# Kernel tuning notes

Hardware: AMD Instinct MI355X
Metric: run time of the kernel (lower is better)

The kernel has to match this reference:

```python
import jax, jax.numpy as jnp
import numpy as np

N = 50000
E = 400000


def _cheb_norm(edge_index, dtype):
    # PyG ChebConv norm (normalization='sym', lambda_max=2.0):
    # remove self loops, L_hat = -D^{-1/2} A D^{-1/2} on off-diagonal edges.
    src, dst = edge_index[0], edge_index[1]
    mask = (src != dst).astype(dtype)
    deg = jax.ops.segment_sum(mask, src, num_segments=N)
    dinv = jnp.where(deg > 0, jax.lax.rsqrt(jnp.where(deg > 0, deg, 1.0)), 0.0)
    w = -dinv[src] * dinv[dst] * mask  # [E]
    return src, dst, w


def _cheb_conv(x, src, dst, w, W0, W1, b):
    # out = T0(x) W0 + T1(x) W1 + b, T0 = x, T1 = L_hat x
    tx1 = jax.ops.segment_sum(w[:, None] * x[src], dst, num_segments=N)
    return x @ W0 + tx1 @ W1 + b


def setup_inputs() -> dict:
    key = jax.random.key(0)
    ks = jax.random.split(key, 12)
    s = 0.05
    inp = {
        "x": jax.random.normal(ks[0], (N, 128), dtype=jnp.float32),
        "edge_index": jax.random.randint(ks[1], (2, E), 0, N, dtype=jnp.int64),
        "W1_0": jax.random.normal(ks[2], (128, 256), dtype=jnp.float32) * s,
        "W1_1": jax.random.normal(ks[3], (128, 256), dtype=jnp.float32) * s,
        "b1": jnp.zeros((256,), dtype=jnp.float32),
        "W2_0": jax.random.normal(ks[4], (256, 256), dtype=jnp.float32) * s,
        "W2_1": jax.random.normal(ks[5], (256, 256), dtype=jnp.float32) * s,
        "b2": jnp.zeros((256,), dtype=jnp.float32),
        "W3_0": jax.random.normal(ks[6], (256, 256), dtype=jnp.float32) * s,
        "W3_1": jax.random.normal(ks[7], (256, 256), dtype=jnp.float32) * s,
        "b3": jnp.zeros((256,), dtype=jnp.float32),
    }
    return inp


def reference(x, edge_index, W1_0, W1_1, b1, W2_0, W2_1, b2, W3_0, W3_1, b3):
    # Eval mode: F.dropout with training=False is identity, so dropout is omitted.
    src, dst, w = _cheb_norm(edge_index, x.dtype)
    h = jax.nn.relu(_cheb_conv(x, src, dst, w, W1_0, W1_1, b1))
    h = jax.nn.relu(_cheb_conv(h, src, dst, w, W2_0, W2_1, b2))
    h = _cheb_conv(h, src, dst, w, W3_0, W3_1, b3)
    return h
```

## Files before the change

### kernel.cpp

```cpp
#include <hip/hip_runtime.h>
#include <hip/hip_bf16.h>


typedef __attribute__((ext_vector_type(8))) short bf16x8;
typedef __attribute__((ext_vector_type(4))) float f32x4;

__device__ __forceinline__ float bf2f(unsigned int lo16) {
    unsigned int t = lo16 << 16;
    return __builtin_bit_cast(float, t);
}
__device__ __forceinline__ unsigned short f2bf(float f) {
    unsigned int u = __builtin_bit_cast(unsigned int, f);
    unsigned int r = (u + 0x7fffu + ((u >> 16) & 1u)) >> 16;
    return (unsigned short)r;
}

__global__ __launch_bounds__(256) void deg_cnt_kernel(const int* __restrict__ src,
                                                      const int* __restrict__ dst,
                                                      float* __restrict__ deg,
                                                      int* __restrict__ cnt, int E) {
    int e = blockIdx.x * blockDim.x + threadIdx.x;
    if (e < E) {
        int s = src[e], d = dst[e];
        if (s != d) atomicAdd(&deg[s], 1.0f);
        atomicAdd(&cnt[d], 1);
    }
}

__global__ __launch_bounds__(256) void dinv_kernel(float* __restrict__ deg, int N) {
    int i = blockIdx.x * blockDim.x + threadIdx.x;
    if (i < N) {
        float d = deg[i];
        deg[i] = (d > 0.0f) ? rsqrtf(d) : 0.0f;
    }
}

__global__ __launch_bounds__(256) void scan_partial(const int* __restrict__ cnt,
                                                    int* __restrict__ part, int N) {
    __shared__ int lds[256];
    int tid = threadIdx.x;
    int base = blockIdx.x * 1024 + tid * 4;
    int s = 0;
    #pragma unroll
    for (int i = 0; i < 4; ++i) if (base + i < N) s += cnt[base + i];
    lds[tid] = s;
    __syncthreads();
    for (int off = 128; off > 0; off >>= 1) {
        if (tid < off) lds[tid] += lds[tid + off];
        __syncthreads();
    }
    if (tid == 0) part[blockIdx.x] = lds[0];
}

__global__ __launch_bounds__(64) void scan_small(int* __restrict__ part, int NB,
                                                 int* __restrict__ rowptr, int N) {
    if (threadIdx.x == 0 && blockIdx.x == 0) {
        int total = 0;
        for (int i = 0; i < NB; ++i) { int t = part[i]; part[i] = total; total += t; }
        rowptr[N] = total;
    }
}

__global__ __launch_bounds__(256) void scan_chunk(const int* __restrict__ cnt,
                                                  const int* __restrict__ part,
                                                  int* __restrict__ rowptr, int N) {
    __shared__ int lds[256];
    int tid = threadIdx.x;
    int base = blockIdx.x * 1024 + tid * 4;
    int c[4];
    #pragma unroll
    for (int i = 0; i < 4; ++i) c[i] = (base + i < N) ? cnt[base + i] : 0;
    int ts = c[0] + c[1] + c[2] + c[3];
    lds[tid] = ts;
    __syncthreads();
    for (int off = 1; off < 256; off <<= 1) {
        int v = (tid >= off) ? lds[tid - off] : 0;
        __syncthreads();
        lds[tid] += v;
        __syncthreads();
    }
    int o = part[blockIdx.x] + lds[tid] - ts;
    #pragma unroll
    for (int i = 0; i < 4; ++i) {
        if (base + i < N) rowptr[base + i] = o;
        o += c[i];
    }
}

__global__ __launch_bounds__(256) void fill_kernel(const int* __restrict__ src,
                                                   const int* __restrict__ dst,
                                                   const float* __restrict__ dinv,
                                                   int* __restrict__ cursor,
                                                   int* __restrict__ esrc,
                                                   float* __restrict__ ew, int E) {
    int e = blockIdx.x * blockDim.x + threadIdx.x;
    if (e < E) {
        int s = src[e], d = dst[e];
        int pos = atomicAdd(&cursor[d], 1);
        esrc[pos] = s;
        ew[pos] = (s != d) ? (-dinv[s] * dinv[d]) : 0.0f;
    }
}

__global__ __launch_bounds__(256) void cast_x_kernel(const float* __restrict__ x,
                                                     unsigned short* __restrict__ xb,
                                                     long long n4) {
    long long i = (long long)blockIdx.x * 256 + threadIdx.x;
    if (i >= n4) return;
    float4 v = reinterpret_cast<const float4*>(x)[i];
    ushort4 o;
    o.x = f2bf(v.x); o.y = f2bf(v.y); o.z = f2bf(v.z); o.w = f2bf(v.w);
    reinterpret_cast<ushort4*>(xb)[i] = o;
}

struct TParams {
    const float* W[6];
    unsigned short* WT[6];
    int K[6];
};
__global__ __launch_bounds__(256) void transpose_cast_all(TParams p) {
    int m = blockIdx.z;
    int K = p.K[m];
    int kb = blockIdx.x * 32, nb = blockIdx.y * 32;
    if (kb >= K) return;
    const float* W = p.W[m];
    unsigned short* WT = p.WT[m];
    __shared__ float t[32][33];
    int lx = threadIdx.x & 31, ly = threadIdx.x >> 5;
    #pragma unroll
    for (int i = 0; i < 32; i += 8)
        t[ly + i][lx] = W[(size_t)(kb + ly + i) * 256 + nb + lx];
    __syncthreads();
    #pragma unroll
    for (int i = 0; i < 32; i += 8)
        WT[(size_t)(nb + ly + i) * K + kb + lx] = f2bf(t[lx][ly + i]);
}

template <int F>
__global__ __launch_bounds__(256) void gather_bf16(const int* __restrict__ rowptr,
                                                   const int* __restrict__ esrc,
                                                   const float* __restrict__ ew,
                                                   const unsigned short* __restrict__ xb,
                                                   unsigned short* __restrict__ txb,
                                                   int N) {
    constexpr int V = F / 64;
    int wave = threadIdx.x >> 6, lane = threadIdx.x & 63;
    int n = blockIdx.x * 4 + wave;
    if (n >= N) return;
    int beg = rowptr[n], end = rowptr[n + 1];
    float acc[V] = {};
    int s_next = 0; float w_next = 0.0f;
    if (beg < end) { s_next = esrc[beg]; w_next = ew[beg]; }
    for (int k = beg; k < end; ++k) {
        int s = s_next; float wv = w_next;
        if (k + 1 < end) { s_next = esrc[k + 1]; w_next = ew[k + 1]; }
        const unsigned short* p = &xb[(size_t)s * F + lane * V];
        if (V == 2) {
            unsigned int u = *reinterpret_cast<const unsigned int*>(p);
            acc[0] += wv * bf2f(u & 0xffffu);
            acc[1] += wv * bf2f(u >> 16);
        } else {
            uint2 u = *reinterpret_cast<const uint2*>(p);
            acc[0] += wv * bf2f(u.x & 0xffffu);
            acc[1] += wv * bf2f(u.x >> 16);
            acc[2] += wv * bf2f(u.y & 0xffffu);
            acc[3] += wv * bf2f(u.y >> 16);
        }
    }
    unsigned short* q = &txb[(size_t)n * F + lane * V];
    if (V == 2) {
        unsigned int o = (unsigned int)f2bf(acc[0]) | ((unsigned int)f2bf(acc[1]) << 16);
        *reinterpret_cast<unsigned int*>(q) = o;
    } else {
        uint2 o;
        o.x = (unsigned int)f2bf(acc[0]) | ((unsigned int)f2bf(acc[1]) << 16);
        o.y = (unsigned int)f2bf(acc[2]) | ((unsigned int)f2bf(acc[3]) << 16);
        *reinterpret_cast<uint2*>(q) = o;
    }
}

template <int K, bool RELU, typename OutT>
__global__ __launch_bounds__(256, 3) void gemm_mfma(const unsigned short* __restrict__ Xb,
                                                    const unsigned short* __restrict__ Tb,
                                                    const unsigned short* __restrict__ W0T,
                                                    const unsigned short* __restrict__ W1T,
                                                    const float* __restrict__ bias,
                                                    OutT* __restrict__ out, int M) {
    constexpr int SA = 72;
    __shared__ unsigned short As[64 * SA];
    __shared__ unsigned short Bs[256 * SA];

    const int tid = threadIdx.x;
    const int wave = tid >> 6;
    const int lane = tid & 63;
    const int l15 = lane & 15;
    const int quad = lane >> 4;
    const int row0 = blockIdx.x * 64;

    const int srow = tid >> 3;
    const int scol = (tid & 7) * 8;

    f32x4 acc[4][4];
    #pragma unroll
    for (int i = 0; i < 4; ++i)
        #pragma unroll
        for (int j = 0; j < 4; ++j) acc[i][j] = (f32x4){0.f, 0.f, 0.f, 0.f};

    #pragma unroll
    for (int pass = 0; pass < 2; ++pass) {
        const unsigned short* Amat = pass ? Tb : Xb;
        const unsigned short* Wmat = pass ? W1T : W0T;
        for (int k0 = 0; k0 < K; k0 += 64) {
            if (pass != 0 || k0 != 0) __syncthreads();
            #pragma unroll
            for (int r = 0; r < 2; ++r) {
                int row = r * 32 + srow;
                int grow = row0 + row; if (grow > M - 1) grow = M - 1;
                uint4 v = *reinterpret_cast<const uint4*>(&Amat[(size_t)grow * K + k0 + scol]);
                *reinterpret_cast<uint4*>(&As[row * SA + scol]) = v;
            }
            #pragma unroll
            for (int r = 0; r < 8; ++r) {
                int row = r * 32 + srow;
                uint4 v = *reinterpret_cast<const uint4*>(&Wmat[(size_t)row * K + k0 + scol]);
                *reinterpret_cast<uint4*>(&Bs[row * SA + scol]) = v;
            }
            __syncthreads();

            #pragma unroll
            for (int kf = 0; kf < 2; ++kf) {
                const int koff = kf * 32 + quad * 8;
                bf16x8 a[4], b[4];
                #pragma unroll
                for (int mt = 0; mt < 4; ++mt)
                    a[mt] = *reinterpret_cast<const bf16x8*>(&As[(mt * 16 + l15) * SA + koff]);
                #pragma unroll
                for (int nt = 0; nt < 4; ++nt)
                    b[nt] = *reinterpret_cast<const bf16x8*>(
                        &Bs[(wave * 64 + nt * 16 + l15) * SA + koff]);
                #pragma unroll
                for (int mt = 0; mt < 4; ++mt)
                    #pragma unroll
                    for (int nt = 0; nt < 4; ++nt)
                        acc[mt][nt] = __builtin_amdgcn_mfma_f32_16x16x32_bf16(
                            a[mt], b[nt], acc[mt][nt], 0, 0, 0);
            }
        }
    }

    #pragma unroll
    for (int mt = 0; mt < 4; ++mt) {
        #pragma unroll
        for (int r = 0; r < 4; ++r) {
            int m = row0 + mt * 16 + quad * 4 + r;
            if (m >= M) continue;
            #pragma unroll
            for (int nt = 0; nt < 4; ++nt) {
                int n = wave * 64 + nt * 16 + l15;
                float v = acc[mt][nt][r] + bias[n];
                if (RELU) v = fmaxf(v, 0.0f);
                if constexpr (sizeof(OutT) == 2)
                    out[(size_t)m * 256 + n] = (OutT)f2bf(v);
                else
                    out[(size_t)m * 256 + n] = (OutT)v;
            }
        }
    }
}

static inline size_t align_up(size_t v, size_t a) { return (v + a - 1) / a * a; }

extern "C" void kernel_launch(void* const* d_in, const int* in_sizes, int n_in,
                              void* d_out, int out_size, void* d_ws, size_t ws_size,
                              hipStream_t stream) {
    const float* x    = (const float*)d_in[0];
    const int*   ei   = (const int*)d_in[1];
    const float* W1_0 = (const float*)d_in[2];
    const float* W1_1 = (const float*)d_in[3];
    const float* b1   = (const float*)d_in[4];
    const float* W2_0 = (const float*)d_in[5];
    const float* W2_1 = (const float*)d_in[6];
    const float* b2   = (const float*)d_in[7];
    const float* W3_0 = (const float*)d_in[8];
    const float* W3_1 = (const float*)d_in[9];
    const float* b3   = (const float*)d_in[10];
    float* out = (float*)d_out;

    const int N = in_sizes[0] / 128;
    const int E = in_sizes[1] / 2;
    const int* src = ei;
    const int* dst = ei + E;

    typedef unsigned short u16;
    char* ws = (char*)d_ws;
    size_t off = 0;
    float* dinv   = (float*)(ws + off); off = align_up(off + (size_t)N * 4, 256);
    int*   cnt    = (int*)  (ws + off); off = align_up(off + (size_t)N * 4, 256);
    size_t zero_end = off;
    int*   rowptr = (int*)  (ws + off); off = align_up(off + (size_t)(N + 1) * 4, 256);
    int*   cursor = (int*)  (ws + off); off = align_up(off + (size_t)N * 4, 256);
    int*   part   = (int*)  (ws + off); off = align_up(off + 256 * 4, 256);
    int*   esrc   = (int*)  (ws + off); off = align_up(off + (size_t)E * 4, 256);
    float* ew     = (float*)(ws + off); off = align_up(off + (size_t)E * 4, 256);
    u16*   xb     = (u16*)  (ws + off); off = align_up(off + (size_t)N * 128 * 2, 256);
    u16*   txb    = (u16*)  (ws + off); off = align_up(off + (size_t)N * 256 * 2, 256);
    u16*   h1b    = (u16*)  (ws + off); off = align_up(off + (size_t)N * 256 * 2, 256);
    u16*   h2b    = (u16*)  (ws + off); off = align_up(off + (size_t)N * 256 * 2, 256);
    u16*   W10T   = (u16*)  (ws + off); off = align_up(off + (size_t)256 * 128 * 2, 256);
    u16*   W11T   = (u16*)  (ws + off); off = align_up(off + (size_t)256 * 128 * 2, 256);
    u16*   W20T   = (u16*)  (ws + off); off = align_up(off + (size_t)256 * 256 * 2, 256);
    u16*   W21T   = (u16*)  (ws + off); off = align_up(off + (size_t)256 * 256 * 2, 256);
    u16*   W30T   = (u16*)  (ws + off); off = align_up(off + (size_t)256 * 256 * 2, 256);
    u16*   W31T   = (u16*)  (ws + off); off = align_up(off + (size_t)256 * 256 * 2, 256);
    (void)ws_size;

    const int TB = 256;
    dim3 gE((E + TB - 1) / TB);
    dim3 gN((N + TB - 1) / TB);
    const int NB = (N + 1023) / 1024;

    hipMemsetAsync(dinv, 0, zero_end, stream);
    deg_cnt_kernel<<<gE, TB, 0, stream>>>(src, dst, dinv, cnt, E);
    dinv_kernel<<<gN, TB, 0, stream>>>(dinv, N);
    scan_partial<<<NB, 256, 0, stream>>>(cnt, part, N);
    scan_small<<<1, 64, 0, stream>>>(part, NB, rowptr, N);
    scan_chunk<<<NB, 256, 0, stream>>>(cnt, part, rowptr, N);
    hipMemcpyAsync(cursor, rowptr, (size_t)N * 4, hipMemcpyDeviceToDevice, stream);
    fill_kernel<<<gE, TB, 0, stream>>>(src, dst, dinv, cursor, esrc, ew, E);

    {
        long long n4 = (long long)N * 128 / 4;
        cast_x_kernel<<<(unsigned)((n4 + 255) / 256), TB, 0, stream>>>(x, xb, n4);
    }
    {
        TParams p;
        p.W[0] = W1_0; p.WT[0] = W10T; p.K[0] = 128;
        p.W[1] = W1_1; p.WT[1] = W11T; p.K[1] = 128;
        p.W[2] = W2_0; p.WT[2] = W20T; p.K[2] = 256;
        p.W[3] = W2_1; p.WT[3] = W21T; p.K[3] = 256;
        p.W[4] = W3_0; p.WT[4] = W30T; p.K[4] = 256;
        p.W[5] = W3_1; p.WT[5] = W31T; p.K[5] = 256;
        transpose_cast_all<<<dim3(8, 8, 6), TB, 0, stream>>>(p);
    }

    dim3 gemmGrid((N + 63) / 64);
    dim3 gatherGrid((N + 3) / 4);

    gather_bf16<128><<<gatherGrid, TB, 0, stream>>>(rowptr, esrc, ew, xb, txb, N);
    gemm_mfma<128, true, u16><<<gemmGrid, TB, 0, stream>>>(xb, txb, W10T, W11T, b1, h1b, N);

    gather_bf16<256><<<gatherGrid, TB, 0, stream>>>(rowptr, esrc, ew, h1b, txb, N);
    gemm_mfma<256, true, u16><<<gemmGrid, TB, 0, stream>>>(h1b, txb, W20T, W21T, b2, h2b, N);

    gather_bf16<256><<<gatherGrid, TB, 0, stream>>>(rowptr, esrc, ew, h2b, txb, N);
    gemm_mfma<256, false, float><<<gemmGrid, TB, 0, stream>>>(h2b, txb, W30T, W31T, b3, out, N);
}
```

Baseline: 372.0 us.

## Fuse neighbor gather into MFMA GEMM via shared-memory aggregated tile

Each layer's sparse aggregation is now computed inside the GEMM kernel: every block gathers its 64 destination rows into an LDS tile and feeds the second MFMA pass directly from that tile, so the bf16 intermediate no longer goes to global memory. The dinv computation is folded into the partial scan, and the cursor copy is folded into the chunk scan, which removes two launches and a memcpy. In exchange, LDS use per block grows (occupancy hint lowered from 3 to 2), and the gather runs serially per wave before the GEMM, with no overlap across blocks except through occupancy.

```diff
diff --git a/kernel.cpp b/kernel.cpp
--- a/kernel.cpp
+++ b/kernel.cpp
@@ -27,22 +27,21 @@
     }
 }
 
-__global__ __launch_bounds__(256) void dinv_kernel(float* __restrict__ deg, int N) {
-    int i = blockIdx.x * blockDim.x + threadIdx.x;
-    if (i < N) {
-        float d = deg[i];
-        deg[i] = (d > 0.0f) ? rsqrtf(d) : 0.0f;
-    }
-}
-
-__global__ __launch_bounds__(256) void scan_partial(const int* __restrict__ cnt,
-                                                    int* __restrict__ part, int N) {
+__global__ __launch_bounds__(256) void scan_partial_dinv(const int* __restrict__ cnt,
+                                                         int* __restrict__ part,
+                                                         float* __restrict__ deg, int N) {
     __shared__ int lds[256];
     int tid = threadIdx.x;
     int base = blockIdx.x * 1024 + tid * 4;
     int s = 0;
     #pragma unroll
-    for (int i = 0; i < 4; ++i) if (base + i < N) s += cnt[base + i];
+    for (int i = 0; i < 4; ++i) {
+        if (base + i < N) {
+            s += cnt[base + i];
+            float d = deg[base + i];
+            deg[base + i] = (d > 0.0f) ? rsqrtf(d) : 0.0f;
+        }
+    }
     lds[tid] = s;
     __syncthreads();
     for (int off = 128; off > 0; off >>= 1) {
@@ -63,7 +62,8 @@
 
 __global__ __launch_bounds__(256) void scan_chunk(const int* __restrict__ cnt,
                                                   const int* __restrict__ part,
-                                                  int* __restrict__ rowptr, int N) {
+                                                  int* __restrict__ rowptr,
+                                                  int* __restrict__ cursor, int N) {
     __shared__ int lds[256];
     int tid = threadIdx.x;
     int base = blockIdx.x * 1024 + tid * 4;
@@ -82,7 +82,7 @@
     int o = part[blockIdx.x] + lds[tid] - ts;
     #pragma unroll
     for (int i = 0; i < 4; ++i) {
-        if (base + i < N) rowptr[base + i] = o;
+        if (base + i < N) { rowptr[base + i] = o; cursor[base + i] = o; }
         o += c[i];
     }
 }
@@ -136,57 +136,18 @@
         WT[(size_t)(nb + ly + i) * K + kb + lx] = f2bf(t[lx][ly + i]);
 }
 
-template <int F>
-__global__ __launch_bounds__(256) void gather_bf16(const int* __restrict__ rowptr,
-                                                   const int* __restrict__ esrc,
-                                                   const float* __restrict__ ew,
-                                                   const unsigned short* __restrict__ xb,
-                                                   unsigned short* __restrict__ txb,
-                                                   int N) {
-    constexpr int V = F / 64;
-    int wave = threadIdx.x >> 6, lane = threadIdx.x & 63;
-    int n = blockIdx.x * 4 + wave;
-    if (n >= N) return;
-    int beg = rowptr[n], end = rowptr[n + 1];
-    float acc[V] = {};
-    int s_next = 0; float w_next = 0.0f;
-    if (beg < end) { s_next = esrc[beg]; w_next = ew[beg]; }
-    for (int k = beg; k < end; ++k) {
-        int s = s_next; float wv = w_next;
-        if (k + 1 < end) { s_next = esrc[k + 1]; w_next = ew[k + 1]; }
-        const unsigned short* p = &xb[(size_t)s * F + lane * V];
-        if (V == 2) {
-            unsigned int u = *reinterpret_cast<const unsigned int*>(p);
-            acc[0] += wv * bf2f(u & 0xffffu);
-            acc[1] += wv * bf2f(u >> 16);
-        } else {
-            uint2 u = *reinterpret_cast<const uint2*>(p);
-            acc[0] += wv * bf2f(u.x & 0xffffu);
-            acc[1] += wv * bf2f(u.x >> 16);
-            acc[2] += wv * bf2f(u.y & 0xffffu);
-            acc[3] += wv * bf2f(u.y >> 16);
-        }
-    }
-    unsigned short* q = &txb[(size_t)n * F + lane * V];
-    if (V == 2) {
-        unsigned int o = (unsigned int)f2bf(acc[0]) | ((unsigned int)f2bf(acc[1]) << 16);
-        *reinterpret_cast<unsigned int*>(q) = o;
-    } else {
-        uint2 o;
-        o.x = (unsigned int)f2bf(acc[0]) | ((unsigned int)f2bf(acc[1]) << 16);
-        o.y = (unsigned int)f2bf(acc[2]) | ((unsigned int)f2bf(acc[3]) << 16);
-        *reinterpret_cast<uint2*>(q) = o;
-    }
-}
-
 template <int K, bool RELU, typename OutT>
-__global__ __launch_bounds__(256, 3) void gemm_mfma(const unsigned short* __restrict__ Xb,
-                                                    const unsigned short* __restrict__ Tb,
-                                                    const unsigned short* __restrict__ W0T,
-                                                    const unsigned short* __restrict__ W1T,
-                                                    const float* __restrict__ bias,
-                                                    OutT* __restrict__ out, int M) {
+__global__ __launch_bounds__(256, 2) void layer_fused(const unsigned short* __restrict__ Hb,
+                                                      const int* __restrict__ rowptr,
+                                                      const int* __restrict__ esrc,
+                                                      const float* __restrict__ ew,
+                                                      const unsigned short* __restrict__ W0T,
+                                                      const unsigned short* __restrict__ W1T,
+                                                      const float* __restrict__ bias,
+                                                      OutT* __restrict__ out, int M) {
     constexpr int SA = 72;
+    constexpr int TSS = K + 8;
+    __shared__ unsigned short Ts[64 * TSS];
     __shared__ unsigned short As[64 * SA];
     __shared__ unsigned short Bs[256 * SA];
 
@@ -197,27 +158,65 @@
     const int quad = lane >> 4;
     const int row0 = blockIdx.x * 64;
 
+    constexpr int V = K / 64;
+    for (int i = 0; i < 16; ++i) {
+        int nl = wave * 16 + i;
+        int gn = row0 + nl;
+        int beg = 0, end = 0;
+        if (gn < M) { beg = rowptr[gn]; end = rowptr[gn + 1]; }
+        float acc[V] = {};
+        int s_next = 0; float w_next = 0.0f;
+        if (beg < end) { s_next = esrc[beg]; w_next = ew[beg]; }
+        for (int k = beg; k < end; ++k) {
+            int s = s_next; float wv = w_next;
+            if (k + 1 < end) { s_next = esrc[k + 1]; w_next = ew[k + 1]; }
+            const unsigned short* p = &Hb[(size_t)s * K + lane * V];
+            if (V == 2) {
+                unsigned int u = *reinterpret_cast<const unsigned int*>(p);
+                acc[0] += wv * bf2f(u & 0xffffu);
+                acc[1] += wv * bf2f(u >> 16);
+            } else {
+                uint2 u = *reinterpret_cast<const uint2*>(p);
+                acc[0] += wv * bf2f(u.x & 0xffffu);
+                acc[1] += wv * bf2f(u.x >> 16);
+                acc[2] += wv * bf2f(u.y & 0xffffu);
+                acc[3] += wv * bf2f(u.y >> 16);
+            }
+        }
+        unsigned short* q = &Ts[nl * TSS + lane * V];
+        if (V == 2) {
+            unsigned int o = (unsigned int)f2bf(acc[0]) | ((unsigned int)f2bf(acc[1]) << 16);
+            *reinterpret_cast<unsigned int*>(q) = o;
+        } else {
+            uint2 o;
+            o.x = (unsigned int)f2bf(acc[0]) | ((unsigned int)f2bf(acc[1]) << 16);
+            o.y = (unsigned int)f2bf(acc[2]) | ((unsigned int)f2bf(acc[3]) << 16);
+            *reinterpret_cast<uint2*>(q) = o;
+        }
+    }
+
     const int srow = tid >> 3;
     const int scol = (tid & 7) * 8;
 
-    f32x4 acc[4][4];
+    f32x4 acc4[4][4];
     #pragma unroll
     for (int i = 0; i < 4; ++i)
         #pragma unroll
-        for (int j = 0; j < 4; ++j) acc[i][j] = (f32x4){0.f, 0.f, 0.f, 0.f};
+        for (int j = 0; j < 4; ++j) acc4[i][j] = (f32x4){0.f, 0.f, 0.f, 0.f};
 
     #pragma unroll
     for (int pass = 0; pass < 2; ++pass) {
-        const unsigned short* Amat = pass ? Tb : Xb;
         const unsigned short* Wmat = pass ? W1T : W0T;
         for (int k0 = 0; k0 < K; k0 += 64) {
             if (pass != 0 || k0 != 0) __syncthreads();
-            #pragma unroll
-            for (int r = 0; r < 2; ++r) {
-                int row = r * 32 + srow;
-                int grow = row0 + row; if (grow > M - 1) grow = M - 1;
-                uint4 v = *reinterpret_cast<const uint4*>(&Amat[(size_t)grow * K + k0 + scol]);
-                *reinterpret_cast<uint4*>(&As[row * SA + scol]) = v;
+            if (pass == 0) {
+                #pragma unroll
+                for (int r = 0; r < 2; ++r) {
+                    int row = r * 32 + srow;
+                    int grow = row0 + row; if (grow > M - 1) grow = M - 1;
+                    uint4 v = *reinterpret_cast<const uint4*>(&Hb[(size_t)grow * K + k0 + scol]);
+                    *reinterpret_cast<uint4*>(&As[row * SA + scol]) = v;
+                }
             }
             #pragma unroll
             for (int r = 0; r < 8; ++r) {
@@ -232,8 +231,12 @@
                 const int koff = kf * 32 + quad * 8;
                 bf16x8 a[4], b[4];
                 #pragma unroll
-                for (int mt = 0; mt < 4; ++mt)
-                    a[mt] = *reinterpret_cast<const bf16x8*>(&As[(mt * 16 + l15) * SA + koff]);
+                for (int mt = 0; mt < 4; ++mt) {
+                    if (pass == 0)
+                        a[mt] = *reinterpret_cast<const bf16x8*>(&As[(mt * 16 + l15) * SA + koff]);
+                    else
+                        a[mt] = *reinterpret_cast<const bf16x8*>(&Ts[(mt * 16 + l15) * TSS + k0 + koff]);
+                }
                 #pragma unroll
                 for (int nt = 0; nt < 4; ++nt)
                     b[nt] = *reinterpret_cast<const bf16x8*>(
@@ -242,8 +245,8 @@
                 for (int mt = 0; mt < 4; ++mt)
                     #pragma unroll
                     for (int nt = 0; nt < 4; ++nt)
-                        acc[mt][nt] = __builtin_amdgcn_mfma_f32_16x16x32_bf16(
-                            a[mt], b[nt], acc[mt][nt], 0, 0, 0);
+                        acc4[mt][nt] = __builtin_amdgcn_mfma_f32_16x16x32_bf16(
+                            a[mt], b[nt], acc4[mt][nt], 0, 0, 0);
             }
         }
     }
@@ -257,7 +260,7 @@
             #pragma unroll
             for (int nt = 0; nt < 4; ++nt) {
                 int n = wave * 64 + nt * 16 + l15;
-                float v = acc[mt][nt][r] + bias[n];
+                float v = acc4[mt][nt][r] + bias[n];
                 if (RELU) v = fmaxf(v, 0.0f);
                 if constexpr (sizeof(OutT) == 2)
                     out[(size_t)m * 256 + n] = (OutT)f2bf(v);
@@ -303,7 +306,6 @@
     int*   esrc   = (int*)  (ws + off); off = align_up(off + (size_t)E * 4, 256);
     float* ew     = (float*)(ws + off); off = align_up(off + (size_t)E * 4, 256);
     u16*   xb     = (u16*)  (ws + off); off = align_up(off + (size_t)N * 128 * 2, 256);
-    u16*   txb    = (u16*)  (ws + off); off = align_up(off + (size_t)N * 256 * 2, 256);
     u16*   h1b    = (u16*)  (ws + off); off = align_up(off + (size_t)N * 256 * 2, 256);
     u16*   h2b    = (u16*)  (ws + off); off = align_up(off + (size_t)N * 256 * 2, 256);
     u16*   W10T   = (u16*)  (ws + off); off = align_up(off + (size_t)256 * 128 * 2, 256);
@@ -316,16 +318,13 @@
 
     const int TB = 256;
     dim3 gE((E + TB - 1) / TB);
-    dim3 gN((N + TB - 1) / TB);
     const int NB = (N + 1023) / 1024;
 
     hipMemsetAsync(dinv, 0, zero_end, stream);
     deg_cnt_kernel<<<gE, TB, 0, stream>>>(src, dst, dinv, cnt, E);
-    dinv_kernel<<<gN, TB, 0, stream>>>(dinv, N);
-    scan_partial<<<NB, 256, 0, stream>>>(cnt, part, N);
+    scan_partial_dinv<<<NB, 256, 0, stream>>>(cnt, part, dinv, N);
     scan_small<<<1, 64, 0, stream>>>(part, NB, rowptr, N);
-    scan_chunk<<<NB, 256, 0, stream>>>(cnt, part, rowptr, N);
-    hipMemcpyAsync(cursor, rowptr, (size_t)N * 4, hipMemcpyDeviceToDevice, stream);
+    scan_chunk<<<NB, 256, 0, stream>>>(cnt, part, rowptr, cursor, N);
     fill_kernel<<<gE, TB, 0, stream>>>(src, dst, dinv, cursor, esrc, ew, E);
 
     {
@@ -343,15 +342,12 @@
         transpose_cast_all<<<dim3(8, 8, 6), TB, 0, stream>>>(p);
     }
 
-    dim3 gemmGrid((N + 63) / 64);
-    dim3 gatherGrid((N + 3) / 4);
-
-    gather_bf16<128><<<gatherGrid, TB, 0, stream>>>(rowptr, esrc, ew, xb, txb, N);
-    gemm_mfma<128, true, u16><<<gemmGrid, TB, 0, stream>>>(xb, txb, W10T, W11T, b1, h1b, N);
-
-    gather_bf16<256><<<gatherGrid, TB, 0, stream>>>(rowptr, esrc, ew, h1b, txb, N);
-    gemm_mfma<256, true, u16><<<gemmGrid, TB, 0, stream>>>(h1b, txb, W20T, W21T, b2, h2b, N);
-
-    gather_bf16<256><<<gatherGrid, TB, 0, stream>>>(rowptr, esrc, ew, h2b, txb, N);
-    gemm_mfma<256, false, float><<<gemmGrid, TB, 0, stream>>>(h2b, txb, W30T, W31T, b3, out, N);
-}
+    dim3 grid((N + 63) / 64);
+
+    layer_fused<128, true, u16><<<grid, TB, 0, stream>>>(xb, rowptr, esrc, ew,
+                                                         W10T, W11T, b1, h1b, N);
+    layer_fused<256, true, u16><<<grid, TB, 0, stream>>>(h1b, rowptr, esrc, ew,
+                                                         W20T, W21T, b2, h2b, N);
+    layer_fused<256, false, float><<<grid, TB, 0, stream>>>(h2b, rowptr, esrc, ew,
+                                                            W30T, W31T, b3, out, N);
+}
```

Result: slower. 588.0 us (+58.1%).

## Fuse dinv into scan, drop cursor copy, unroll gather loop by four

Applied to the files above, without the earlier changes.

The rsqrt degree normalization moves into the scan-partial kernel, which removes one launch. The fill kernel now uses rowptr plus an atomic counter that the existing memset zeroes, so the device-to-device cursor copy is no longer needed. The gather loop is unrolled by four with independent row loads to raise memory-level parallelism. In exchange, registers per thread go up slightly and the memset clears a larger region.

```diff
diff --git a/kernel.cpp b/kernel.cpp
--- a/kernel.cpp
+++ b/kernel.cpp
@@ -27,22 +27,21 @@
     }
 }
 
-__global__ __launch_bounds__(256) void dinv_kernel(float* __restrict__ deg, int N) {
-    int i = blockIdx.x * blockDim.x + threadIdx.x;
-    if (i < N) {
-        float d = deg[i];
-        deg[i] = (d > 0.0f) ? rsqrtf(d) : 0.0f;
-    }
-}
-
-__global__ __launch_bounds__(256) void scan_partial(const int* __restrict__ cnt,
-                                                    int* __restrict__ part, int N) {
+__global__ __launch_bounds__(256) void scan_partial_dinv(const int* __restrict__ cnt,
+                                                         int* __restrict__ part,
+                                                         float* __restrict__ deg, int N) {
     __shared__ int lds[256];
     int tid = threadIdx.x;
     int base = blockIdx.x * 1024 + tid * 4;
     int s = 0;
     #pragma unroll
-    for (int i = 0; i < 4; ++i) if (base + i < N) s += cnt[base + i];
+    for (int i = 0; i < 4; ++i) {
+        if (base + i < N) {
+            s += cnt[base + i];
+            float d = deg[base + i];
+            deg[base + i] = (d > 0.0f) ? rsqrtf(d) : 0.0f;
+        }
+    }
     lds[tid] = s;
     __syncthreads();
     for (int off = 128; off > 0; off >>= 1) {
@@ -90,13 +89,14 @@
 __global__ __launch_bounds__(256) void fill_kernel(const int* __restrict__ src,
                                                    const int* __restrict__ dst,
                                                    const float* __restrict__ dinv,
-                                                   int* __restrict__ cursor,
+                                                   const int* __restrict__ rowptr,
+                                                   int* __restrict__ cnt2,
                                                    int* __restrict__ esrc,
                                                    float* __restrict__ ew, int E) {
     int e = blockIdx.x * blockDim.x + threadIdx.x;
     if (e < E) {
         int s = src[e], d = dst[e];
-        int pos = atomicAdd(&cursor[d], 1);
+        int pos = rowptr[d] + atomicAdd(&cnt2[d], 1);
         esrc[pos] = s;
         ew[pos] = (s != d) ? (-dinv[s] * dinv[d]) : 0.0f;
     }
@@ -136,6 +136,21 @@
         WT[(size_t)(nb + ly + i) * K + kb + lx] = f2bf(t[lx][ly + i]);
 }
 
+template <int V> struct RowT;
+template <> struct RowT<2> { using T = unsigned int; };
+template <> struct RowT<4> { using T = uint2; };
+
+__device__ __forceinline__ void fma_row(float* acc, unsigned int u, float wv) {
+    acc[0] += wv * bf2f(u & 0xffffu);
+    acc[1] += wv * bf2f(u >> 16);
+}
+__device__ __forceinline__ void fma_row(float* acc, uint2 u, float wv) {
+    acc[0] += wv * bf2f(u.x & 0xffffu);
+    acc[1] += wv * bf2f(u.x >> 16);
+    acc[2] += wv * bf2f(u.y & 0xffffu);
+    acc[3] += wv * bf2f(u.y >> 16);
+}
+
 template <int F>
 __global__ __launch_bounds__(256) void gather_bf16(const int* __restrict__ rowptr,
                                                    const int* __restrict__ esrc,
@@ -144,29 +159,33 @@
                                                    unsigned short* __restrict__ txb,
                                                    int N) {
     constexpr int V = F / 64;
+    using T = typename RowT<V>::T;
     int wave = threadIdx.x >> 6, lane = threadIdx.x & 63;
     int n = blockIdx.x * 4 + wave;
     if (n >= N) return;
     int beg = rowptr[n], end = rowptr[n + 1];
     float acc[V] = {};
-    int s_next = 0; float w_next = 0.0f;
-    if (beg < end) { s_next = esrc[beg]; w_next = ew[beg]; }
-    for (int k = beg; k < end; ++k) {
-        int s = s_next; float wv = w_next;
-        if (k + 1 < end) { s_next = esrc[k + 1]; w_next = ew[k + 1]; }
-        const unsigned short* p = &xb[(size_t)s * F + lane * V];
-        if (V == 2) {
-            unsigned int u = *reinterpret_cast<const unsigned int*>(p);
-            acc[0] += wv * bf2f(u & 0xffffu);
-            acc[1] += wv * bf2f(u >> 16);
-        } else {
-            uint2 u = *reinterpret_cast<const uint2*>(p);
-            acc[0] += wv * bf2f(u.x & 0xffffu);
-            acc[1] += wv * bf2f(u.x >> 16);
-            acc[2] += wv * bf2f(u.y & 0xffffu);
-            acc[3] += wv * bf2f(u.y >> 16);
-        }
-    }
+
+    int k = beg;
+    for (; k + 4 <= end; k += 4) {
+        int s0 = esrc[k], s1 = esrc[k + 1], s2 = esrc[k + 2], s3 = esrc[k + 3];
+        float w0 = ew[k], w1 = ew[k + 1], w2 = ew[k + 2], w3 = ew[k + 3];
+        T r0 = *reinterpret_cast<const T*>(&xb[(size_t)s0 * F + lane * V]);
+        T r1 = *reinterpret_cast<const T*>(&xb[(size_t)s1 * F + lane * V]);
+        T r2 = *reinterpret_cast<const T*>(&xb[(size_t)s2 * F + lane * V]);
+        T r3 = *reinterpret_cast<const T*>(&xb[(size_t)s3 * F + lane * V]);
+        fma_row(acc, r0, w0);
+        fma_row(acc, r1, w1);
+        fma_row(acc, r2, w2);
+        fma_row(acc, r3, w3);
+    }
+    for (; k < end; ++k) {
+        int s = esrc[k];
+        float wv = ew[k];
+        T r = *reinterpret_cast<const T*>(&xb[(size_t)s * F + lane * V]);
+        fma_row(acc, r, wv);
+    }
+
     unsigned short* q = &txb[(size_t)n * F + lane * V];
     if (V == 2) {
         unsigned int o = (unsigned int)f2bf(acc[0]) | ((unsigned int)f2bf(acc[1]) << 16);
@@ -296,9 +315,9 @@
     size_t off = 0;
     float* dinv   = (float*)(ws + off); off = align_up(off + (size_t)N * 4, 256);
     int*   cnt    = (int*)  (ws + off); off = align_up(off + (size_t)N * 4, 256);
+    int*   cnt2   = (int*)  (ws + off); off = align_up(off + (size_t)N * 4, 256);
     size_t zero_end = off;
     int*   rowptr = (int*)  (ws + off); off = align_up(off + (size_t)(N + 1) * 4, 256);
-    int*   cursor = (int*)  (ws + off); off = align_up(off + (size_t)N * 4, 256);
     int*   part   = (int*)  (ws + off); off = align_up(off + 256 * 4, 256);
     int*   esrc   = (int*)  (ws + off); off = align_up(off + (size_t)E * 4, 256);
     float* ew     = (float*)(ws + off); off = align_up(off + (size_t)E * 4, 256);
@@ -316,17 +335,14 @@
 
     const int TB = 256;
     dim3 gE((E + TB - 1) / TB);
-    dim3 gN((N + TB - 1) / TB);
     const int NB = (N + 1023) / 1024;
 
     hipMemsetAsync(dinv, 0, zero_end, stream);
     deg_cnt_kernel<<<gE, TB, 0, stream>>>(src, dst, dinv, cnt, E);
-    dinv_kernel<<<gN, TB, 0, stream>>>(dinv, N);
-    scan_partial<<<NB, 256, 0, stream>>>(cnt, part, N);
+    scan_partial_dinv<<<NB, 256, 0, stream>>>(cnt, part, dinv, N);
     scan_small<<<1, 64, 0, stream>>>(part, NB, rowptr, N);
     scan_chunk<<<NB, 256, 0, stream>>>(cnt, part, rowptr, N);
-    hipMemcpyAsync(cursor, rowptr, (size_t)N * 4, hipMemcpyDeviceToDevice, stream);
-    fill_kernel<<<gE, TB, 0, stream>>>(src, dst, dinv, cursor, esrc, ew, E);
+    fill_kernel<<<gE, TB, 0, stream>>>(src, dst, dinv, rowptr, cnt2, esrc, ew, E);
 
     {
         long long n4 = (long long)N * 128 / 4;
```

After: 353.4 us. 1.05x faster.
